# Kernel optimization log

Measured on AMD Instinct MI355X. Metric: run time of the kernel, lower is better.

## Reference

```python
import jax, jax.numpy as jnp
import numpy as np

D_MODEL, D_K, D_FF, N = 1024, 128, 4096, 8192

def _linear_params(key, fan_in, fan_out):
    # mimic torch nn.Linear default init (uniform +/- 1/sqrt(fan_in))
    k1, k2 = jax.random.split(key)
    bound = 1.0 / np.sqrt(fan_in)
    W = jax.random.uniform(k1, (fan_out, fan_in), jnp.float32, -bound, bound)
    b = jax.random.uniform(k2, (fan_out,), jnp.float32, -bound, bound)
    return W, b

def setup_inputs() -> dict:
    key = jax.random.key(0)
    ks = jax.random.split(key, 7)
    x = jax.random.normal(ks[0], (N, D_MODEL), jnp.float32)
    Wq, bq = _linear_params(ks[1], D_MODEL, D_K)
    Wk, bk = _linear_params(ks[2], D_MODEL, D_K)
    Wv, bv = _linear_params(ks[3], D_MODEL, D_K)
    Wp, bp = _linear_params(ks[4], D_K, D_MODEL)
    W1, b1 = _linear_params(ks[5], D_MODEL, D_FF)
    W2, b2 = _linear_params(ks[6], D_FF, D_MODEL)
    return {"x": x, "Wq": Wq, "bq": bq, "Wk": Wk, "bk": bk, "Wv": Wv, "bv": bv,
            "Wp": Wp, "bp": bp, "W1": W1, "b1": b1, "W2": W2, "b2": b2}

def reference(x, Wq, bq, Wk, bk, Wv, bv, Wp, bp, W1, b1, W2, b2):
    # projections (torch Linear: x @ W.T + b)
    Q = x @ Wq.T + bq            # [n, d_k]
    K = x @ Wk.T + bk            # [n, d_k]
    V = x @ Wv.T + bv            # [n, d_k]
    # linear attention, original evaluation order: (Q @ K^T) @ V
    attn = Q @ K.T               # [n, n]
    context = attn @ V           # [n, d_k]
    out = context @ Wp.T + bp    # [n, d_model]
    x = x + out                  # residual 1
    h = jax.nn.relu(x @ W1.T + b1)  # [n, d_ff]
    return x + (h @ W2.T + b2)   # residual 2
```

## Files before the change

kernel.cpp:

```cpp
#include <hip/hip_runtime.h>


#define MROWS 8192
#define DMODEL 1024
#define DK 128
#define DFF 4096

typedef __attribute__((ext_vector_type(8))) __bf16 bf16x8;
typedef __attribute__((ext_vector_type(4))) float f32x4;

#define BAR()    __builtin_amdgcn_s_barrier()
#define WAITV(n) asm volatile("s_waitcnt vmcnt(" #n ")" ::: "memory")
#define LGKM0()  asm volatile("s_waitcnt lgkmcnt(0)" ::: "memory")
#define SCHED0() __builtin_amdgcn_sched_barrier(0)
#define GLOAD(src, dst) __builtin_amdgcn_global_load_lds( \
    (const __attribute__((address_space(1))) void*)(src), \
    (__attribute__((address_space(3))) void*)(dst), 16, 0, 0)

#define LDSO(p) ((unsigned)(unsigned long long) \
    (__attribute__((address_space(3))) const char*)(const char*)(p))

__device__ __forceinline__ bf16x8 ldsr(unsigned off) {
    bf16x8 r;
    asm volatile("ds_read_b128 %0, %1" : "=v"(r) : "v"(off));
    return r;
}

__global__ __launch_bounds__(256) void cast_f32_bf16(
    const float* __restrict__ src, __bf16* __restrict__ dst, int n8)
{
    for (int i = blockIdx.x * blockDim.x + threadIdx.x; i < n8;
         i += gridDim.x * blockDim.x) {
        const float4 a = reinterpret_cast<const float4*>(src)[2 * i];
        const float4 b = reinterpret_cast<const float4*>(src)[2 * i + 1];
        bf16x8 o;
        o[0] = (__bf16)a.x; o[1] = (__bf16)a.y; o[2] = (__bf16)a.z; o[3] = (__bf16)a.w;
        o[4] = (__bf16)b.x; o[5] = (__bf16)b.y; o[6] = (__bf16)b.z; o[7] = (__bf16)b.w;
        reinterpret_cast<bf16x8*>(dst)[i] = o;
    }
}

__device__ __forceinline__ void cast_one(const float* s, __bf16* d, int i) {
    const float4 a = reinterpret_cast<const float4*>(s)[2 * i];
    const float4 b = reinterpret_cast<const float4*>(s)[2 * i + 1];
    bf16x8 o;
    o[0] = (__bf16)a.x; o[1] = (__bf16)a.y; o[2] = (__bf16)a.z; o[3] = (__bf16)a.w;
    o[4] = (__bf16)b.x; o[5] = (__bf16)b.y; o[6] = (__bf16)b.z; o[7] = (__bf16)b.w;
    reinterpret_cast<bf16x8*>(d)[i] = o;
}

__global__ __launch_bounds__(256) void cast6(
    const float* __restrict__ s0, __bf16* __restrict__ d0,
    const float* __restrict__ s1, __bf16* __restrict__ d1,
    const float* __restrict__ s2, __bf16* __restrict__ d2,
    const float* __restrict__ s3, __bf16* __restrict__ d3,
    const float* __restrict__ s4, __bf16* __restrict__ d4,
    const float* __restrict__ s5, __bf16* __restrict__ d5)
{
    const int b = blockIdx.x, t = threadIdx.x;
    if      (b <  64)  cast_one(s0, d0, b * 256 + t);
    else if (b < 128)  cast_one(s1, d1, (b - 64) * 256 + t);
    else if (b < 192)  cast_one(s2, d2, (b - 128) * 256 + t);
    else if (b < 256)  cast_one(s3, d3, (b - 192) * 256 + t);
    else if (b < 2304) cast_one(s4, d4, (b - 256) * 256 + t);
    else               cast_one(s5, d5, (b - 2304) * 256 + t);
}

__global__ void pack_bias3(const float* __restrict__ a, const float* __restrict__ b,
                           const float* __restrict__ c, float* __restrict__ o)
{
    const int t = threadIdx.x;
    o[t] = a[t]; o[128 + t] = b[t]; o[256 + t] = c[t];
}

__global__ __launch_bounds__(256) void ffn2_reduce(
    float* __restrict__ y, const __bf16* __restrict__ P0,
    const __bf16* __restrict__ P1, const float* __restrict__ b2, int n8)
{
    for (int i = blockIdx.x * blockDim.x + threadIdx.x; i < n8;
         i += gridDim.x * blockDim.x) {
        const int col0 = (i << 3) & (DMODEL - 1);
        const float4 ba = *reinterpret_cast<const float4*>(&b2[col0]);
        const float4 bb = *reinterpret_cast<const float4*>(&b2[col0 + 4]);
        float4 o0 = reinterpret_cast<const float4*>(y)[2 * i];
        float4 o1 = reinterpret_cast<const float4*>(y)[2 * i + 1];
        const bf16x8 p0 = reinterpret_cast<const bf16x8*>(P0)[i];
        const bf16x8 p1 = reinterpret_cast<const bf16x8*>(P1)[i];
        o0.x += (float)p0[0] + (float)p1[0] + ba.x;
        o0.y += (float)p0[1] + (float)p1[1] + ba.y;
        o0.z += (float)p0[2] + (float)p1[2] + ba.z;
        o0.w += (float)p0[3] + (float)p1[3] + ba.w;
        o1.x += (float)p0[4] + (float)p1[4] + bb.x;
        o1.y += (float)p0[5] + (float)p1[5] + bb.y;
        o1.z += (float)p0[6] + (float)p1[6] + bb.z;
        o1.w += (float)p0[7] + (float)p1[7] + bb.w;
        reinterpret_cast<float4*>(y)[2 * i]     = o0;
        reinterpret_cast<float4*>(y)[2 * i + 1] = o1;
    }
}

template<bool RELU, bool RESID, bool BIAS, bool OUTBF, bool DUAL>
__global__ __launch_bounds__(256) void gemm128(
    const __bf16* __restrict__ A, int lda,
    const __bf16* __restrict__ W,
    const float* __restrict__ bias,
    const float* __restrict__ resid,
    void* __restrict__ Cout, __bf16* __restrict__ Cbf, int ldc, int K)
{
    constexpr int BK = 32;
    __shared__ __bf16 As[128 * BK];
    __shared__ __bf16 Bs[128 * BK];

    const int tid  = threadIdx.x;
    const int lane = tid & 63;
    const int w    = tid >> 6;
    const int wm   = w >> 1;
    const int wn   = w & 1;
    const int fr   = lane & 15;
    const int fq   = lane >> 4;

    const long row0 = (long)blockIdx.y * 128;
    const long col0 = (long)blockIdx.x * 128;

    const int sr = (w << 4) + (lane >> 2);
    const int sc = (lane & 3) << 3;

    const __bf16* gA0 = A + (row0 + sr) * (long)lda + sc;
    const __bf16* gA1 = A + (row0 + 64 + sr) * (long)lda + sc;
    const __bf16* gW0 = W + (col0 + sr) * (long)K + sc;
    const __bf16* gW1 = W + (col0 + 64 + sr) * (long)K + sc;

    __bf16* lA0 = &As[(w << 4) * BK];
    __bf16* lA1 = &As[((w << 4) + 64) * BK];
    __bf16* lB0 = &Bs[(w << 4) * BK];
    __bf16* lB1 = &Bs[((w << 4) + 64) * BK];

    f32x4 acc[4][4] = {};

    for (int k0 = 0; k0 < K; k0 += BK) {
        GLOAD(gA0 + k0, lA0);
        GLOAD(gA1 + k0, lA1);
        GLOAD(gW0 + k0, lB0);
        GLOAD(gW1 + k0, lB1);
        __syncthreads();

        bf16x8 af[4], bfr[4];
        #pragma unroll
        for (int m = 0; m < 4; m++)
            af[m] = *reinterpret_cast<const bf16x8*>(
                &As[(wm * 64 + m * 16 + fr) * BK + fq * 8]);
        #pragma unroll
        for (int n = 0; n < 4; n++)
            bfr[n] = *reinterpret_cast<const bf16x8*>(
                &Bs[(wn * 64 + n * 16 + fr) * BK + fq * 8]);

        #pragma unroll
        for (int m = 0; m < 4; m++)
            #pragma unroll
            for (int n = 0; n < 4; n++)
                acc[m][n] = __builtin_amdgcn_mfma_f32_16x16x32_bf16(
                    af[m], bfr[n], acc[m][n], 0, 0, 0);
        __syncthreads();
    }

    float bc[4];
    #pragma unroll
    for (int n = 0; n < 4; n++)
        bc[n] = BIAS ? bias[col0 + wn * 64 + n * 16 + fr] : 0.0f;
    #pragma unroll
    for (int m = 0; m < 4; m++) {
        #pragma unroll
        for (int j = 0; j < 4; j++) {
            const long r = row0 + wm * 64 + m * 16 + fq * 4 + j;
            #pragma unroll
            for (int n = 0; n < 4; n++) {
                const long c = col0 + wn * 64 + n * 16 + fr;
                float v = acc[m][n][j] + bc[n];
                if constexpr (RESID) v += resid[r * ldc + c];
                if constexpr (RELU)  v = fmaxf(v, 0.0f);
                if constexpr (OUTBF) ((__bf16*)Cout)[r * ldc + c] = (__bf16)v;
                else                 ((float*)Cout)[r * ldc + c] = v;
                if constexpr (DUAL)  Cbf[r * ldc + c] = (__bf16)v;
            }
        }
    }
}

#define RD_B()                                             \
    _Pragma("unroll")                                      \
    for (int n = 0; n < 4; n++) {                          \
        bb[n][0] = ldsr(pB + rb0 + n * 2048);              \
        bb[n][1] = ldsr(pB + rb1 + n * 2048);              \
    }
#define RD_A(m0_, cnt_)                                    \
    _Pragma("unroll")                                      \
    for (int m = m0_; m < m0_ + cnt_; m++) {               \
        a[m][0] = ldsr(pA + rb0 + m * 2048);               \
        a[m][1] = ldsr(pA + rb1 + m * 2048);               \
    }
#define MFMA2(m0_)                                                            \
    _Pragma("unroll")                                                         \
    for (int m = m0_; m < m0_ + 2; m++)                                       \
        _Pragma("unroll")                                                     \
        for (int n = 0; n < 4; n++) {                                         \
            acc[m][n] = __builtin_amdgcn_mfma_f32_16x16x32_bf16(              \
                a[m][0], bb[n][0], acc[m][n], 0, 0, 0);                       \
            acc[m][n] = __builtin_amdgcn_mfma_f32_16x16x32_bf16(              \
                a[m][1], bb[n][1], acc[m][n], 0, 0, 0);                       \
        }

template<bool RELU, bool BIAS>
__global__ __launch_bounds__(512, 2) void gemm256p(
    const __bf16* __restrict__ A, int lda,
    const __bf16* __restrict__ W, int ldw,
    const float* __restrict__ bias,
    __bf16* __restrict__ Cout, long sstride, int ldc,
    int klen, int nb, int nbx)
{
    __shared__ char lds[8][16384];

    const int bid = blockIdx.x;
    const int sid = bid / nb;
    const int ib  = bid % nb;
    const int chunk = nb >> 3;
    const int swz   = (ib & 7) * chunk + (ib >> 3);
    const int bx    = swz % nbx;
    const int by    = swz / nbx;

    const long row0 = (long)by * 256;
    const long col0 = (long)bx * 256;

    const __bf16* Ash = A + (long)sid * klen;
    const __bf16* Wsh = W + (long)sid * klen;

    const int tid  = threadIdx.x;
    const int lane = tid & 63;
    const int w    = tid >> 6;
    const int wm   = w >> 2;
    const int wn   = w & 3;
    const int fr   = lane & 15;
    const int fq   = lane >> 4;

    const int srow8 = lane >> 3;
    const int scole = ((lane & 7) ^ srow8) << 3;
    const __bf16* gA = Ash + (row0 + w * 8 + srow8) * (long)lda + scole;
    const __bf16* gB = Wsh + (col0 + w * 8 + srow8) * (long)ldw + scole;

    char* ldsc = &lds[0][0];
    const unsigned lbase = LDSO(ldsc);
    const int nt = klen >> 6;

    auto stage = [&](int u, int j) {
        if (u >= nt) return;
        char* dst = ldsc + (((u & 1) << 2 | j) << 14) + (w << 10);
        if (j < 2) {
            const __bf16* s = gB + ((long)j * 128) * (long)ldw + (long)u * 64;
            GLOAD(s, dst);
            GLOAD(s + 64 * (long)ldw, dst + 8192);
        } else {
            const __bf16* s = gA + ((long)(j - 2) * 128) * (long)lda + (long)u * 64;
            GLOAD(s, dst);
            GLOAD(s + 64 * (long)lda, dst + 8192);
        }
    };

    const unsigned rb0 = fr * 128 + ((fq * 16) ^ ((fr & 7) << 4));
    const unsigned rb1 = fr * 128 + ((64 + fq * 16) ^ ((fr & 7) << 4));

    f32x4 acc[8][4] = {};
    bf16x8 a[8][2], bb[4][2];

    stage(0, 0); stage(0, 1); stage(0, 2); stage(0, 3);
    stage(1, 0); stage(1, 1); stage(1, 2); stage(1, 3);
    WAITV(8);
    BAR();

    for (int t = 0; t < nt; ++t) {
        const unsigned base = lbase + ((t & 1) << 16);
        const unsigned pB = base + ((wn >> 1) << 14) + ((wn & 1) << 13);
        const unsigned pA = base + ((2 + wm) << 14);

        RD_B(); RD_A(0, 2);
        BAR();
        LGKM0(); SCHED0();
        __builtin_amdgcn_s_setprio(1); MFMA2(0); __builtin_amdgcn_s_setprio(0);
        BAR();
        RD_A(2, 4);
        stage(t + 2, 0); stage(t + 2, 1);
        BAR();
        LGKM0(); SCHED0();
        __builtin_amdgcn_s_setprio(1); MFMA2(2); __builtin_amdgcn_s_setprio(0);
        BAR();
        RD_A(6, 2);
        BAR();
        SCHED0();
        __builtin_amdgcn_s_setprio(1); MFMA2(4); __builtin_amdgcn_s_setprio(0);
        LGKM0();
        BAR();
        stage(t + 2, 2); stage(t + 2, 3);
        SCHED0();
        __builtin_amdgcn_s_setprio(1); MFMA2(6); __builtin_amdgcn_s_setprio(0);
        if (t + 2 < nt)      { WAITV(8); }
        else if (t + 1 < nt) { WAITV(0); }
        BAR();
    }

    __bf16* Cb = Cout + (long)sid * sstride;
    float bc[4];
    #pragma unroll
    for (int n = 0; n < 4; n++)
        bc[n] = BIAS ? bias[col0 + wn * 64 + n * 16 + fr] : 0.0f;

    __bf16* sw = reinterpret_cast<__bf16*>(ldsc) + (w << 13);
    #pragma unroll
    for (int m = 0; m < 8; m++)
        #pragma unroll
        for (int j = 0; j < 4; j++) {
            const int row = m * 16 + fq * 4 + j;
            #pragma unroll
            for (int n = 0; n < 4; n++) {
                float v = acc[m][n][j] + bc[n];
                if constexpr (RELU) v = fmaxf(v, 0.0f);
                sw[row * 64 + n * 16 + fr] = (__bf16)v;
            }
        }
    const long crow0 = row0 + wm * 128;
    const long ccol0 = col0 + wn * 64;
    #pragma unroll
    for (int i = 0; i < 16; i++) {
        const bf16x8 vv = *reinterpret_cast<const bf16x8*>(sw + i * 512 + lane * 8);
        const int r  = i * 8 + (lane >> 3);
        const int cg = (lane & 7) << 3;
        *reinterpret_cast<bf16x8*>(&Cb[(crow0 + r) * (long)ldc + ccol0 + cg]) = vv;
    }
}

__global__ __launch_bounds__(256) void ktv_partial(
    const __bf16* __restrict__ Kp, const __bf16* __restrict__ Vp,
    int ld, float* __restrict__ part)
{
    __shared__ float ks[32][DK];
    __shared__ float vs[32][DK];
    const int tid = threadIdx.x;
    const int ti  = tid >> 4;
    const int tj  = tid & 15;
    float acc[8][8] = {};
    const long base = (long)blockIdx.x * 128;

    for (int n0 = 0; n0 < 128; n0 += 32) {
        for (int t = tid; t < 512; t += 256) {
            const int r  = t >> 4;
            const int cc = (t & 15) << 3;
            const bf16x8 k8 = *reinterpret_cast<const bf16x8*>(
                &Kp[(base + n0 + r) * (long)ld + cc]);
            const bf16x8 v8 = *reinterpret_cast<const bf16x8*>(
                &Vp[(base + n0 + r) * (long)ld + cc]);
            #pragma unroll
            for (int u = 0; u < 8; u++) {
                ks[r][cc + u] = (float)k8[u];
                vs[r][cc + u] = (float)v8[u];
            }
        }
        __syncthreads();
        for (int n = 0; n < 32; n++) {
            float kk[8], vv[8];
            #pragma unroll
            for (int i = 0; i < 8; i++) kk[i] = ks[n][(ti << 3) + i];
            #pragma unroll
            for (int j = 0; j < 8; j++) vv[j] = vs[n][(tj << 3) + j];
            #pragma unroll
            for (int i = 0; i < 8; i++)
                #pragma unroll
                for (int j = 0; j < 8; j++)
                    acc[i][j] = fmaf(kk[i], vv[j], acc[i][j]);
        }
        __syncthreads();
    }

    float* dst = &part[(long)blockIdx.x * (DK * DK)];
    #pragma unroll
    for (int i = 0; i < 8; i++) {
        const int ig = (ti << 3) + i;
        *reinterpret_cast<float4*>(&dst[ig * DK + (tj << 3)]) =
            make_float4(acc[i][0], acc[i][1], acc[i][2], acc[i][3]);
        *reinterpret_cast<float4*>(&dst[ig * DK + (tj << 3) + 4]) =
            make_float4(acc[i][4], acc[i][5], acc[i][6], acc[i][7]);
    }
}

__global__ __launch_bounds__(256) void ktv_reduce(
    const float* __restrict__ part, __bf16* __restrict__ ktvT)
{
    const int t = blockIdx.x * 256 + threadIdx.x;
    const int i = t >> 7;
    const int j = t & 127;
    float s = 0.0f;
    for (int b = 0; b < 64; b++) s += part[(long)b * (DK * DK) + t];
    ktvT[j * DK + i] = (__bf16)s;
}

extern "C" void kernel_launch(void* const* d_in, const int* in_sizes, int n_in,
                              void* d_out, int out_size, void* d_ws, size_t ws_size,
                              hipStream_t stream) {
    const float* x  = (const float*)d_in[0];
    const float* Wq = (const float*)d_in[1];
    const float* bq = (const float*)d_in[2];
    const float* Wk = (const float*)d_in[3];
    const float* bk = (const float*)d_in[4];
    const float* Wv = (const float*)d_in[5];
    const float* bv = (const float*)d_in[6];
    const float* Wp = (const float*)d_in[7];
    const float* bp = (const float*)d_in[8];
    const float* W1 = (const float*)d_in[9];
    const float* b1 = (const float*)d_in[10];
    const float* W2 = (const float*)d_in[11];
    const float* b2 = (const float*)d_in[12];
    float* out = (float*)d_out;

    char* ws = (char*)d_ws;
    const size_t MB = 1ull << 20;
    __bf16* xb    = (__bf16*)(ws);
    __bf16* P0    = (__bf16*)(ws);
    __bf16* P1    = P0 + (long)MROWS * DMODEL;
    __bf16* x2b   = (__bf16*)(ws +  34 * MB);
    __bf16* Hb    = (__bf16*)(ws +  51 * MB);
    __bf16* QKVb  = (__bf16*)(ws + 119 * MB);
    __bf16* W1b   = (__bf16*)(ws + 126 * MB);
    __bf16* W2b   = (__bf16*)(ws + 135 * MB);
    __bf16* Wqkvb = (__bf16*)(ws + 144 * MB);
    __bf16* Wpb   = (__bf16*)(ws + 145 * MB);
    float*  Part  = (float*) (ws + 146 * MB);
    __bf16* KtvTb = (__bf16*)(ws + 151 * MB);
    __bf16* Ctxb  = (__bf16*)(ws + 152 * MB);
    float*  bqkvf = (float*) (ws + 155 * MB);

    const dim3 blk(256);

    cast_f32_bf16<<<2048, blk, 0, stream>>>(x, xb, MROWS * DMODEL / 8);
    cast6<<<4352, blk, 0, stream>>>(
        Wq, Wqkvb, Wk, Wqkvb + DK * DMODEL, Wv, Wqkvb + 2 * DK * DMODEL,
        Wp, Wpb, W1, W1b, W2, W2b);
    pack_bias3<<<1, 128, 0, stream>>>(bq, bk, bv, bqkvf);

    gemm128<false,false,true,true,false><<<dim3(3, 64), blk, 0, stream>>>(
        xb, DMODEL, Wqkvb, bqkvf, nullptr, QKVb, nullptr, 3 * DK, DMODEL);

    ktv_partial<<<64, blk, 0, stream>>>(QKVb + DK, QKVb + 2 * DK, 3 * DK, Part);
    ktv_reduce <<<64, blk, 0, stream>>>(Part, KtvTb);

    gemm128<false,false,false,true,false><<<dim3(1, 64), blk, 0, stream>>>(
        QKVb, 3 * DK, KtvTb, nullptr, nullptr, Ctxb, nullptr, DK, DK);

    gemm128<false,true,true,false,true><<<dim3(8, 64), blk, 0, stream>>>(
        Ctxb, DK, Wpb, bp, x, out, x2b, DMODEL, DK);

    gemm256p<true,true><<<512, 512, 0, stream>>>(
        x2b, DMODEL, W1b, DMODEL, b1, Hb, 0, DFF, DMODEL, 512, DFF / 256);

    gemm256p<false,false><<<256, 512, 0, stream>>>(
        Hb, DFF, W2b, DFF, nullptr, P0,
        (long)MROWS * DMODEL, DMODEL, DFF / 2, 128, DMODEL / 256);

    ffn2_reduce<<<2048, blk, 0, stream>>>(out, P0, P1, b2, MROWS * DMODEL / 8);
}
```

Measured before the change: 240.9 us.

## Software-pipeline LDS fragment reads with double-buffered B registers in gemm256p

```diff
diff --git a/kernel.cpp b/kernel.cpp
--- a/kernel.cpp
+++ b/kernel.cpp
@@ -9,10 +9,10 @@
 typedef __attribute__((ext_vector_type(8))) __bf16 bf16x8;
 typedef __attribute__((ext_vector_type(4))) float f32x4;
 
-#define BAR()    __builtin_amdgcn_s_barrier()
-#define WAITV(n) asm volatile("s_waitcnt vmcnt(" #n ")" ::: "memory")
-#define LGKM0()  asm volatile("s_waitcnt lgkmcnt(0)" ::: "memory")
-#define SCHED0() __builtin_amdgcn_sched_barrier(0)
+#define BAR()     __builtin_amdgcn_s_barrier()
+#define WAITV(n)  asm volatile("s_waitcnt vmcnt(" #n ")" ::: "memory")
+#define LGKMC(n)  asm volatile("s_waitcnt lgkmcnt(" #n ")" ::: "memory")
+#define SCHED0()  __builtin_amdgcn_sched_barrier(0)
 #define GLOAD(src, dst) __builtin_amdgcn_global_load_lds( \
     (const __attribute__((address_space(1))) void*)(src), \
     (__attribute__((address_space(3))) void*)(dst), 16, 0, 0)
@@ -186,28 +186,58 @@
     }
 }
 
-#define RD_B()                                             \
-    _Pragma("unroll")                                      \
-    for (int n = 0; n < 4; n++) {                          \
-        bb[n][0] = ldsr(pB + rb0 + n * 2048);              \
-        bb[n][1] = ldsr(pB + rb1 + n * 2048);              \
-    }
-#define RD_A(m0_, cnt_)                                    \
-    _Pragma("unroll")                                      \
-    for (int m = m0_; m < m0_ + cnt_; m++) {               \
-        a[m][0] = ldsr(pA + rb0 + m * 2048);               \
-        a[m][1] = ldsr(pA + rb1 + m * 2048);               \
-    }
-#define MFMA2(m0_)                                                            \
+#define RD_Q(q, pa, mb_)                                  \
+    q[0][0] = ldsr((pa) + rb0 + (mb_) * 2048);            \
+    q[0][1] = ldsr((pa) + rb1 + (mb_) * 2048);            \
+    q[1][0] = ldsr((pa) + rb0 + ((mb_) + 1) * 2048);      \
+    q[1][1] = ldsr((pa) + rb1 + ((mb_) + 1) * 2048);
+
+#define RD_BB(bset, pb)                                   \
+    _Pragma("unroll")                                     \
+    for (int n = 0; n < 4; n++) {                         \
+        bset[n][0] = ldsr((pb) + rb0 + n * 2048);         \
+        bset[n][1] = ldsr((pb) + rb1 + n * 2048);         \
+    }
+
+#define MFMAQ(q, bset, mb_)                                                   \
     _Pragma("unroll")                                                         \
-    for (int m = m0_; m < m0_ + 2; m++)                                       \
+    for (int i = 0; i < 2; i++)                                               \
         _Pragma("unroll")                                                     \
         for (int n = 0; n < 4; n++) {                                         \
-            acc[m][n] = __builtin_amdgcn_mfma_f32_16x16x32_bf16(              \
-                a[m][0], bb[n][0], acc[m][n], 0, 0, 0);                       \
-            acc[m][n] = __builtin_amdgcn_mfma_f32_16x16x32_bf16(              \
-                a[m][1], bb[n][1], acc[m][n], 0, 0, 0);                       \
-        }
+            acc[(mb_) + i][n] = __builtin_amdgcn_mfma_f32_16x16x32_bf16(      \
+                q[i][0], bset[n][0], acc[(mb_) + i][n], 0, 0, 0);             \
+            acc[(mb_) + i][n] = __builtin_amdgcn_mfma_f32_16x16x32_bf16(      \
+                q[i][1], bset[n][1], acc[(mb_) + i][n], 0, 0, 0);             \
+        }
+
+#define TILE(t, BBC, BBN)                                                     \
+  {                                                                           \
+    const unsigned pA  = lbase + (((t) & 1) << 16) + ((2 + wm) << 14);        \
+    const unsigned pAn = lbase + ((((t) + 1) & 1) << 16) + ((2 + wm) << 14);  \
+    const unsigned pBn = lbase + ((((t) + 1) & 1) << 16)                      \
+                         + ((wn >> 1) << 14) + ((wn & 1) << 13);              \
+    RD_Q(q1, pA, 2);                                                          \
+    LGKMC(4); SCHED0();                                                       \
+    __builtin_amdgcn_s_setprio(1); MFMAQ(q0, BBC, 0);                         \
+    __builtin_amdgcn_s_setprio(0); SCHED0();                                  \
+    RD_Q(q0, pA, 4);                                                          \
+    LGKMC(4); SCHED0();                                                       \
+    __builtin_amdgcn_s_setprio(1); MFMAQ(q1, BBC, 2);                         \
+    __builtin_amdgcn_s_setprio(0); SCHED0();                                  \
+    RD_Q(q1, pA, 6);                                                          \
+    LGKMC(4); SCHED0();                                                       \
+    __builtin_amdgcn_s_setprio(1); MFMAQ(q0, BBC, 4);                         \
+    __builtin_amdgcn_s_setprio(0); SCHED0();                                  \
+    WAITV(0);                                                                 \
+    LGKMC(0);                                                                 \
+    BAR();                                                                    \
+    stage((t) + 2, 0); stage((t) + 2, 1);                                     \
+    stage((t) + 2, 2); stage((t) + 2, 3);                                     \
+    if ((t) + 1 < nt) { RD_BB(BBN, pBn); RD_Q(q0, pAn, 0); }                  \
+    SCHED0();                                                                 \
+    __builtin_amdgcn_s_setprio(1); MFMAQ(q1, BBC, 6);                         \
+    __builtin_amdgcn_s_setprio(0); SCHED0();                                  \
+  }
 
 template<bool RELU, bool BIAS>
 __global__ __launch_bounds__(512, 2) void gemm256p(
@@ -268,41 +298,22 @@
     const unsigned rb1 = fr * 128 + ((64 + fq * 16) ^ ((fr & 7) << 4));
 
     f32x4 acc[8][4] = {};
-    bf16x8 a[8][2], bb[4][2];
+    bf16x8 q0[2][2], q1[2][2], bbA[4][2], bbB[4][2];
 
     stage(0, 0); stage(0, 1); stage(0, 2); stage(0, 3);
     stage(1, 0); stage(1, 1); stage(1, 2); stage(1, 3);
     WAITV(8);
     BAR();
-
-    for (int t = 0; t < nt; ++t) {
-        const unsigned base = lbase + ((t & 1) << 16);
-        const unsigned pB = base + ((wn >> 1) << 14) + ((wn & 1) << 13);
-        const unsigned pA = base + ((2 + wm) << 14);
-
-        RD_B(); RD_A(0, 2);
-        BAR();
-        LGKM0(); SCHED0();
-        __builtin_amdgcn_s_setprio(1); MFMA2(0); __builtin_amdgcn_s_setprio(0);
-        BAR();
-        RD_A(2, 4);
-        stage(t + 2, 0); stage(t + 2, 1);
-        BAR();
-        LGKM0(); SCHED0();
-        __builtin_amdgcn_s_setprio(1); MFMA2(2); __builtin_amdgcn_s_setprio(0);
-        BAR();
-        RD_A(6, 2);
-        BAR();
-        SCHED0();
-        __builtin_amdgcn_s_setprio(1); MFMA2(4); __builtin_amdgcn_s_setprio(0);
-        LGKM0();
-        BAR();
-        stage(t + 2, 2); stage(t + 2, 3);
-        SCHED0();
-        __builtin_amdgcn_s_setprio(1); MFMA2(6); __builtin_amdgcn_s_setprio(0);
-        if (t + 2 < nt)      { WAITV(8); }
-        else if (t + 1 < nt) { WAITV(0); }
-        BAR();
+    {
+        const unsigned pB0 = lbase + ((wn >> 1) << 14) + ((wn & 1) << 13);
+        const unsigned pA0 = lbase + ((2 + wm) << 14);
+        RD_BB(bbA, pB0);
+        RD_Q(q0, pA0, 0);
+    }
+
+    for (int tt = 0; tt < nt; tt += 2) {
+        TILE(tt,     bbA, bbB)
+        TILE(tt + 1, bbB, bbA)
     }
 
     __bf16* Cb = Cout + (long)sid * sstride;
```

After: 369.1 us. 53.2% more time.
